# Optimization experiments

Hardware: AMD Instinct MI355X
Metric: run time of the kernel (lower is better)

Reference implementation:

```python
import jax, jax.numpy as jnp
import numpy as np

N_WAY = 5
K_SHOT = 1
QUERY = 75          # queries per class -> 375 total
PRJ = 14            # projections per support class
C, H, W = 512, 10, 10
NUM_NODE = H * W
SINK_EPS = 0.05     # entropic regularization (on max-normalized cost)
SINK_ITERS = 50


def setup_inputs() -> dict:
    key = jax.random.key(0)
    k1, k2 = jax.random.split(key)
    n_support = N_WAY * K_SHOT * PRJ
    num_query = N_WAY * QUERY
    feat = jax.random.normal(k1, (n_support + num_query, C, H, W), dtype=jnp.float32)
    label = jax.random.randint(k2, (num_query,), 0, N_WAY)
    return {"feat": feat, "label": label}


def _sinkhorn(cost, r, c, eps=SINK_EPS, iters=SINK_ITERS):
    """Batched entropic OT (log-domain Sinkhorn), replacing the per-pair
    cv2.EMD CPU solve. cost: [..., n, m]; r: [..., n]; c: [..., m].
    r and c each sum to NUM_NODE, so total transported mass is NUM_NODE,
    matching the cv2.EMD flow scale. Scaling the cost by a positive scalar
    does not change the (exact-)OT plan, so we max-normalize per pair for a
    consistent effective regularization."""
    scale = jnp.max(cost, axis=(-1, -2), keepdims=True) + 1e-6
    cost = cost / scale
    log_r = jnp.log(r)
    log_c = jnp.log(c)

    def body(fg, _):
        f, g = fg
        f = eps * (log_r - jax.nn.logsumexp((g[..., None, :] - cost) / eps, axis=-1))
        g = eps * (log_c - jax.nn.logsumexp((f[..., :, None] - cost) / eps, axis=-2))
        return (f, g), None

    init = (jnp.zeros_like(r), jnp.zeros_like(c))
    (f, g), _ = jax.lax.scan(body, init, None, length=iters)
    return jnp.exp((f[..., :, None] + g[..., None, :] - cost) / eps)


def reference(feat, label):
    n_support = N_WAY * K_SHOT * PRJ
    support = feat[:n_support].reshape(N_WAY, PRJ, C, H, W)
    query = feat[n_support:]                       # [nq, C, H, W]
    proto = support.mean(axis=1)                   # [way, C, H, W]
    nq = query.shape[0]

    # --- get_weight_vector: <A_node_feat, global_avg(B)> per (A,B) pair ---
    proto_avg = proto.mean(axis=(2, 3))            # [way, C]
    query_avg = query.mean(axis=(2, 3))            # [nq, C]
    qf = query.reshape(nq, C, NUM_NODE)
    pf = proto.reshape(N_WAY, C, NUM_NODE)
    w1 = jax.nn.relu(jnp.einsum('mcp,nc->mnp', qf, proto_avg)) + 0.001  # [nq, way, N]
    w2 = jax.nn.relu(jnp.einsum('ncp,mc->nmp', pf, query_avg)) + 0.001  # [way, nq, N]

    # --- normalize_feature: subtract channel mean ---
    protoN = proto - proto.mean(axis=1, keepdims=True)
    queryN = query - query.mean(axis=1, keepdims=True)

    # --- similarity map: 1 - squared L2 over channels, per node pair ---
    p = protoN.reshape(N_WAY, C, NUM_NODE).transpose(0, 2, 1)  # [way, N, C]
    q = queryN.reshape(nq, C, NUM_NODE).transpose(0, 2, 1)     # [nq, N, C]
    qn = (q ** 2).sum(-1)                                      # [nq, N]
    pn = (p ** 2).sum(-1)                                      # [way, N]
    cross = jnp.einsum('iac,jbc->ijab', q, p)                  # [nq, way, N, N]
    sqd = qn[:, None, :, None] + pn[None, :, None, :] - 2.0 * cross
    sim = 1.0 - sqd                                            # similarity_map
    cost = sqd                                                 # = 1 - sim

    # --- marginal weights, normalized to sum NUM_NODE (as in emd_inference) ---
    ww1 = jax.nn.relu(w1) + 1e-5
    ww1 = ww1 * (NUM_NODE / ww1.sum(-1, keepdims=True))        # [nq, way, N]
    ww2 = jax.nn.relu(jnp.transpose(w2, (1, 0, 2))) + 1e-5     # weight_2[j,i] -> [nq, way, N]
    ww2 = ww2 * (NUM_NODE / ww2.sum(-1, keepdims=True))

    # --- OT flow (detached, like torch.from_numpy(flow)) ---
    flow = jax.lax.stop_gradient(
        _sinkhorn(jax.lax.stop_gradient(cost), jax.lax.stop_gradient(ww1), jax.lax.stop_gradient(ww2))
    )

    temperature = 12.5 / NUM_NODE
    logits = (sim * flow).sum((-1, -2)) * temperature          # [nq, way]
    log_p_y = jax.nn.log_softmax(logits, axis=1)
    loss = -jnp.take_along_axis(log_p_y, label[:, None], axis=1).mean()
    return (log_p_y, loss)
```

## Files before the change

### kernel.cpp

```cpp
#include <hip/hip_runtime.h>
#include <math.h>

#define NW   5
#define PRJ  14
#define CCH  512
#define PP   100
#define NQ   375
#define NS   70
#define NPAIR (NQ*NW)

#define OFF_PROTO   0
#define OFF_PAVG    256000
#define OFF_QAVG    258560
#define OFF_QSQ     450560
#define OFF_PSQ     488060
#define OFF_LOGITS  488560
#define OFF_PF16    490440
#define OFF_AUX     654280
#define OFF_KG      1036780
#define OFF_QF16    19786844
#define REQ1_WS_BYTES ((size_t)(OFF_KG + 18750000 + 64) * 4)
#define REQ2_WS_BYTES ((size_t)(OFF_QF16 + 12288000 + 64) * 4)

typedef float f32x16 __attribute__((ext_vector_type(16)));
typedef _Float16 f16x2 __attribute__((ext_vector_type(2)));
typedef _Float16 f16x8 __attribute__((ext_vector_type(8)));

__device__ __forceinline__ int SWZ(int n) { return n ^ ((n >> 2) & 7); }

__global__ void k_proto(const float* __restrict__ feat, float* __restrict__ ws) {
    int nc = blockIdx.x;
    int n  = nc >> 9;
    int p  = threadIdx.x;
    float s = 0.f;
    if (p < PP) {
        const float* base = feat + (size_t)((n * PRJ) * CCH) * PP + (size_t)(nc & 511) * PP + p;
        #pragma unroll
        for (int k = 0; k < PRJ; ++k) s += base[(size_t)k * CCH * PP];
        s *= (1.f / PRJ);
        ws[OFF_PROTO + nc * PP + p] = s;
    }
    float v = (p < PP) ? s : 0.f;
    #pragma unroll
    for (int off = 32; off; off >>= 1) v += __shfl_down(v, off);
    __shared__ float red[2];
    if ((threadIdx.x & 63) == 0) red[threadIdx.x >> 6] = v;
    __syncthreads();
    if (threadIdx.x == 0) ws[OFF_PAVG + nc] = (red[0] + red[1]) * (1.f / PP);
}

__global__ __launch_bounds__(256) void k_qstat(const float* __restrict__ src,
                                               float* __restrict__ dst_sq,
                                               float* __restrict__ dst_avg) {
    __shared__ __align__(16) float t[6400];
    int b = blockIdx.x, tid = threadIdx.x;
    const float* base = src + (size_t)b * CCH * PP;
    float qsq = 0.f;
    for (int c0 = 0; c0 < CCH; c0 += 64) {
        __syncthreads();
        const float4* g = (const float4*)(base + (size_t)c0 * PP);
        for (int i = tid; i < 1600; i += 256) ((float4*)t)[i] = g[i];
        __syncthreads();
        if (tid < PP) {
            #pragma unroll 8
            for (int c = 0; c < 64; ++c) { float x = t[c * PP + tid]; qsq = fmaf(x, x, qsq); }
        } else if (tid >= 128 && tid < 192) {
            int ch = tid - 128;
            const float4* row = (const float4*)(t + ch * PP);
            float s = 0.f;
            #pragma unroll
            for (int i = 0; i < 25; ++i) { float4 v = row[i]; s += (v.x + v.y) + (v.z + v.w); }
            if (dst_avg) dst_avg[(size_t)b * CCH + c0 + ch] = s * (1.f / PP);
        }
    }
    if (tid < PP) dst_sq[b * PP + tid] = qsq;
}

__global__ __launch_bounds__(256) void k_conv(const float* __restrict__ src,
                                              const float* __restrict__ avg,
                                              uint* __restrict__ dst) {
    int b = blockIdx.x;
    int id = b >> 4, kt = b & 15;
    int tid = threadIdx.x;
    int c0 = kt * 32;
    uint* img = dst + (size_t)b * 2048;
    const float* pb = src + (size_t)id * CCH * PP;
    const float* pavg = avg + (size_t)id * CCH;
    for (int i = tid; i < 1600; i += 256) {
        int cp = i / 100, col = i - cp * 100;
        float a0 = pb[(size_t)(c0 + 2 * cp) * PP + col];
        float a1 = pb[(size_t)(c0 + 2 * cp + 1) * PP + col];
        uint pk = __builtin_bit_cast(uint, __builtin_amdgcn_cvt_pkrtz(a0, a1));
        img[(((cp >> 2) << 7) | SWZ(col)) * 4 + (cp & 3)] = pk;
    }
    if (tid < 16) {
        int cp = tid;
        float a0 = pavg[c0 + 2 * cp], a1 = pavg[c0 + 2 * cp + 1];
        uint pk = __builtin_bit_cast(uint, __builtin_amdgcn_cvt_pkrtz(a0, a1));
        img[(((cp >> 2) << 7) | 101) * 4 + (cp & 3)] = pk;
    }
    for (int i = tid; i < 448; i += 256) {
        int dw = i & 3; int t2 = i >> 2;
        int s_i = t2 % 28; int k4 = t2 / 28;
        int s = 100 + s_i;
        if (s == 101) continue;
        img[(((k4) << 7) | s) * 4 + dw] = (s == 100) ? 0x3C003C00u : 0u;
    }
}


__global__ __launch_bounds__(256, 4) void k_cost2(float* __restrict__ ws) {
    __shared__ __align__(16) char SH[22400];
    __shared__ float wrL[PP], wcL[PP], qnl[PP], pnl[PP], sqv[PP], spv[PP];
    __shared__ float red[8];
    uint* Kst = (uint*)SH;

    int p_ = blockIdx.x;
    int xcd = p_ & 7, off_ = p_ >> 3;
    int pair = (xcd < 3) ? (xcd * 235 + off_) : (705 + (xcd - 3) * 234 + off_);

    int m = pair / NW;
    int n = pair - m * NW;
    int tid = threadIdx.x;
    int lane = tid & 63, wid = tid >> 6;
    int lrow = lane & 31, lhi = lane >> 5;

    const char* qimg = (const char*)((const uint*)(ws + OFF_QF16) + (size_t)m * 16 * 2048);
    const char* pimg = (const char*)((const uint*)(ws + OFF_PF16) + (size_t)n * 16 * 2048);

    f32x16 acc[4];
    #pragma unroll
    for (int tc = 0; tc < 4; ++tc)
        #pragma unroll
        for (int e = 0; e < 16; ++e) acc[tc][e] = 0.f;

    int arow16 = SWZ(32 * wid + lrow) * 16;
    int bcol16[4];
    #pragma unroll
    for (int tc = 0; tc < 4; ++tc) bcol16[tc] = SWZ(32 * tc + lrow) * 16;

    #pragma unroll 2
    for (int kt = 0; kt < 16; ++kt) {
        const char* qk = qimg + kt * 8192;
        const char* pk = pimg + kt * 8192;
        #pragma unroll
        for (int s = 0; s < 2; ++s) {
            int kb = (2 * s + lhi) * 2048;
            f16x8 ah = *(const f16x8*)(qk + kb + arow16);
            f16x8 b0 = *(const f16x8*)(pk + kb + bcol16[0]);
            f16x8 b1 = *(const f16x8*)(pk + kb + bcol16[1]);
            f16x8 b2 = *(const f16x8*)(pk + kb + bcol16[2]);
            f16x8 b3 = *(const f16x8*)(pk + kb + bcol16[3]);
            acc[0] = __builtin_amdgcn_mfma_f32_32x32x16_f16(ah, b0, acc[0], 0, 0, 0);
            acc[1] = __builtin_amdgcn_mfma_f32_32x32x16_f16(ah, b1, acc[1], 0, 0, 0);
            acc[2] = __builtin_amdgcn_mfma_f32_32x32x16_f16(ah, b2, acc[2], 0, 0, 0);
            acc[3] = __builtin_amdgcn_mfma_f32_32x32x16_f16(ah, b3, acc[3], 0, 0, 0);
        }
    }

    if ((lane & 31) == 4 || (lane & 31) == 5) {
        float* dst = ((lane & 31) == 4) ? wrL : sqv;
        #pragma unroll
        for (int reg = 0; reg < 16; ++reg) {
            int row = 32 * wid + (reg & 3) + 8 * (reg >> 2) + 4 * lhi;
            if (row < PP) dst[row] = acc[3][reg];
        }
    }
    if (wid == 3 && lhi == 1) {
        #pragma unroll
        for (int tc = 0; tc < 4; ++tc) {
            int col = 32 * tc + lrow;
            if (col < PP) { wcL[col] = acc[tc][0]; spv[col] = acc[tc][1]; }
        }
    }
    __syncthreads();

    float v1 = 0.f, v2 = 0.f;
    if (tid < PP) {
        v1 = fmaxf(wrL[tid], 0.f) + 0.00101f;
        v2 = fmaxf(wcL[tid], 0.f) + 0.00101f;
    }
    float s1 = v1, s2 = v2;
    #pragma unroll
    for (int off = 32; off; off >>= 1) { s1 += __shfl_down(s1, off); s2 += __shfl_down(s2, off); }
    if ((tid & 63) == 0) { red[tid >> 6] = s1; red[4 + (tid >> 6)] = s2; }
    __syncthreads();
    float t1 = red[0] + red[1], t2 = red[4] + red[5];
    if (tid < PP) {
        wrL[tid] = v1 * (100.f / t1) * 4.f;
        wcL[tid] = v2 * (100.f / t2) * 4.f;
        float sq = sqv[tid], sp = spv[tid];
        qnl[tid] = ws[OFF_QSQ + m * PP + tid] - sq * sq * (1.f / 512.f);
        pnl[tid] = ws[OFF_PSQ + n * PP + tid] - sp * sp * (1.f / 512.f);
    }
    __syncthreads();

    float spc[4], pnc[4];
    #pragma unroll
    for (int tc = 0; tc < 4; ++tc) {
        int col = 32 * tc + lrow;
        bool cv = col < PP;
        spc[tc] = cv ? spv[col] : 0.f;
        pnc[tc] = cv ? pnl[col] : 0.f;
    }
    float mymax = -1e30f;
    #pragma unroll
    for (int reg = 0; reg < 16; ++reg) {
        int row = 32 * wid + (reg & 3) + 8 * (reg >> 2) + 4 * lhi;
        bool rv = row < PP;
        float sqr = rv ? sqv[row] : 0.f;
        float qnr = rv ? qnl[row] : 0.f;
        #pragma unroll
        for (int tc = 0; tc < 4; ++tc) {
            float sqd = qnr + pnc[tc] - 2.f * (acc[tc][reg] - sqr * spc[tc] * (1.f / 512.f));
            acc[tc][reg] = sqd;
            int col = 32 * tc + lrow;
            if (rv && col < PP) mymax = fmaxf(mymax, sqd);
        }
    }
    #pragma unroll
    for (int off = 32; off; off >>= 1) mymax = fmaxf(mymax, __shfl_down(mymax, off));
    __syncthreads();
    if (lane == 0) red[wid] = mymax;
    __syncthreads();
    float scale = fmaxf(fmaxf(red[0], red[1]), fmaxf(red[2], red[3])) + 1e-6f;
    float k2 = (1.f / scale) * (20.f * 1.44269504088896f);

    #pragma unroll
    for (int tc = 0; tc < 4; ++tc) {
        float kv[16];
        #pragma unroll
        for (int reg = 0; reg < 16; ++reg) kv[reg] = exp2f(fmaf(-acc[tc][reg], k2, 15.f));
        int col = 32 * tc + lrow;
        #pragma unroll
        for (int reg = 0; reg < 16; ++reg) {
            float pv = __shfl_xor(kv[reg], 1);
            int row = 32 * wid + (reg & 3) + 8 * (reg >> 2) + 4 * lhi;
            if (!(lane & 1) && row < PP && col < PP) {
                int j = col >> 1;
                int dw = (j < 25) ? j : (j + 3);
                uint pk = __builtin_bit_cast(uint, __builtin_amdgcn_cvt_pkrtz(kv[reg], pv));
                Kst[row * 56 + dw] = pk;
            }
        }
    }
    __syncthreads();

    int r_ = tid >> 1, hf = tid & 1;
    bool sact = tid < 200;
    if (sact) {
        uint Kr[25], KTr[25];
        const uint* rp = Kst + r_ * 56 + 28 * hf;
        #pragma unroll
        for (int q = 0; q < 25; ++q) Kr[q] = rp[q];
        int j = r_ >> 1;
        int dwc = (j < 25) ? j : (j + 3);
        int sh = (r_ & 1) * 16;
        const uint* cp0 = Kst + (50 * hf) * 56 + dwc;
        #pragma unroll
        for (int q = 0; q < 25; ++q) {
            uint d0 = cp0[(2 * q) * 56];
            uint d1 = cp0[(2 * q + 1) * 56];
            KTr[q] = ((d0 >> sh) & 0xFFFFu) | (((d1 >> sh) & 0xFFFFu) << 16);
        }
        uint* kg = (uint*)(ws + OFF_KG) + (size_t)pair * 10000 + (r_ >> 1);
        int ibR = (r_ & 1) * 50 + 25 * hf;
        int ibT = 100 + (r_ & 1) * 50 + 25 * hf;
        #pragma unroll
        for (int q = 0; q < 25; ++q) kg[(ibR + q) * 50] = Kr[q];
        #pragma unroll
        for (int q = 0; q < 25; ++q) kg[(ibT + q) * 50] = KTr[q];
    }
    float* aux = ws + OFF_AUX + (size_t)pair * 204;
    if (tid < PP) { aux[tid] = wrL[tid]; aux[100 + tid] = wcL[tid]; }
    if (tid == 0) aux[200] = scale;
}

__global__ __launch_bounds__(256, 4) void k_costL(const float* __restrict__ query,
                                                  float* __restrict__ ws) {
    __shared__ __align__(16) char SH[22400];
    __shared__ float wrL[PP], wcL[PP], qnl[PP], pnl[PP], sqv[PP], spv[PP];
    __shared__ float red[8];
    uint* Kst = (uint*)SH;

    int p_ = blockIdx.x;
    int xcd = p_ & 7, off_ = p_ >> 3;
    int pair = (xcd < 3) ? (xcd * 235 + off_) : (705 + (xcd - 3) * 234 + off_);

    int m = pair / NW;
    int n = pair - m * NW;
    int tid = threadIdx.x;
    int lane = tid & 63, wid = tid >> 6;
    int lrow = lane & 31, lhi = lane >> 5;

    const float* qb = query + (size_t)m * CCH * PP;
    const float* qavg_g = ws + OFF_QAVG + (size_t)m * CCH;
    const uint* pimg = (const uint*)(ws + OFF_PF16) + (size_t)n * 16 * 2048;

    for (int idx = tid; idx < 112; idx += 256) {
        int s_i = idx % 28; int k4 = idx / 28;
        int s = 100 + s_i;
        if (s == 101) continue;
        uint4 val = (s == 100)
                  ? make_uint4(0x3C003C00u, 0x3C003C00u, 0x3C003C00u, 0x3C003C00u)
                  : make_uint4(0u, 0u, 0u, 0u);
        *(uint4*)&SH[(k4 * 128 + s) * 16] = val;
    }

    f32x16 acc[4];
    #pragma unroll
    for (int tc = 0; tc < 4; ++tc)
        #pragma unroll
        for (int e = 0; e < 16; ++e) acc[tc][e] = 0.f;

    int arow16 = SWZ(32 * wid + lrow) * 16;
    int bcol16[4];
    #pragma unroll
    for (int tc = 0; tc < 4; ++tc) bcol16[tc] = SWZ(32 * tc + lrow) * 16;

    for (int kt = 0; kt < 16; ++kt) {
        int c0 = kt * 32;
        for (int idx = tid; idx < 400; idx += 256) {
            int cp = idx / 25, n4 = idx - cp * 25;
            const float* src = qb + (size_t)(c0 + 2 * cp) * PP + n4 * 4;
            float4 x0 = *(const float4*)src;
            float4 x1 = *(const float4*)(src + PP);
            const float* p0 = (const float*)&x0;
            const float* p1 = (const float*)&x1;
            int basedw = ((cp >> 2) << 7);
            int dwb = (cp & 3) * 4;
            #pragma unroll
            for (int i4 = 0; i4 < 4; ++i4) {
                int node = n4 * 4 + i4;
                uint pk = __builtin_bit_cast(uint, __builtin_amdgcn_cvt_pkrtz(p0[i4], p1[i4]));
                *(uint*)&SH[(basedw + SWZ(node)) * 16 + dwb] = pk;
            }
        }
        if (tid < 16) {
            int cp = tid;
            uint pk = __builtin_bit_cast(uint,
                __builtin_amdgcn_cvt_pkrtz(qavg_g[c0 + 2 * cp], qavg_g[c0 + 2 * cp + 1]));
            *(uint*)&SH[(((cp >> 2) << 7) + 101) * 16 + (cp & 3) * 4] = pk;
        }
        {
            const float4* gB = (const float4*)(pimg + (size_t)kt * 2048);
            float4* sB = (float4*)&SH[8192];
            for (int i = tid; i < 512; i += 256) sB[i] = gB[i];
        }
        __syncthreads();
        __builtin_amdgcn_s_setprio(1);
        #pragma unroll
        for (int s = 0; s < 2; ++s) {
            int kb = (2 * s + lhi) * 2048;
            f16x8 ah = *(const f16x8*)&SH[kb + arow16];
            #pragma unroll
            for (int tc = 0; tc < 4; ++tc) {
                f16x8 bh = *(const f16x8*)&SH[8192 + kb + bcol16[tc]];
                acc[tc] = __builtin_amdgcn_mfma_f32_32x32x16_f16(ah, bh, acc[tc], 0, 0, 0);
            }
        }
        __builtin_amdgcn_s_setprio(0);
        __syncthreads();
    }

    if ((lane & 31) == 4 || (lane & 31) == 5) {
        float* dst = ((lane & 31) == 4) ? wrL : sqv;
        #pragma unroll
        for (int reg = 0; reg < 16; ++reg) {
            int row = 32 * wid + (reg & 3) + 8 * (reg >> 2) + 4 * lhi;
            if (row < PP) dst[row] = acc[3][reg];
        }
    }
    if (wid == 3 && lhi == 1) {
        #pragma unroll
        for (int tc = 0; tc < 4; ++tc) {
            int col = 32 * tc + lrow;
            if (col < PP) { wcL[col] = acc[tc][0]; spv[col] = acc[tc][1]; }
        }
    }
    __syncthreads();

    float v1 = 0.f, v2 = 0.f;
    if (tid < PP) {
        v1 = fmaxf(wrL[tid], 0.f) + 0.00101f;
        v2 = fmaxf(wcL[tid], 0.f) + 0.00101f;
    }
    float s1 = v1, s2 = v2;
    #pragma unroll
    for (int off = 32; off; off >>= 1) { s1 += __shfl_down(s1, off); s2 += __shfl_down(s2, off); }
    if ((tid & 63) == 0) { red[tid >> 6] = s1; red[4 + (tid >> 6)] = s2; }
    __syncthreads();
    float t1 = red[0] + red[1], t2 = red[4] + red[5];
    if (tid < PP) {
        wrL[tid] = v1 * (100.f / t1) * 4.f;
        wcL[tid] = v2 * (100.f / t2) * 4.f;
        float sq = sqv[tid], sp = spv[tid];
        qnl[tid] = ws[OFF_QSQ + m * PP + tid] - sq * sq * (1.f / 512.f);
        pnl[tid] = ws[OFF_PSQ + n * PP + tid] - sp * sp * (1.f / 512.f);
    }
    __syncthreads();

    float spc[4], pnc[4];
    #pragma unroll
    for (int tc = 0; tc < 4; ++tc) {
        int col = 32 * tc + lrow;
        bool cv = col < PP;
        spc[tc] = cv ? spv[col] : 0.f;
        pnc[tc] = cv ? pnl[col] : 0.f;
    }
    float mymax = -1e30f;
    #pragma unroll
    for (int reg = 0; reg < 16; ++reg) {
        int row = 32 * wid + (reg & 3) + 8 * (reg >> 2) + 4 * lhi;
        bool rv = row < PP;
        float sqr = rv ? sqv[row] : 0.f;
        float qnr = rv ? qnl[row] : 0.f;
        #pragma unroll
        for (int tc = 0; tc < 4; ++tc) {
            float sqd = qnr + pnc[tc] - 2.f * (acc[tc][reg] - sqr * spc[tc] * (1.f / 512.f));
            acc[tc][reg] = sqd;
            int col = 32 * tc + lrow;
            if (rv && col < PP) mymax = fmaxf(mymax, sqd);
        }
    }
    #pragma unroll
    for (int off = 32; off; off >>= 1) mymax = fmaxf(mymax, __shfl_down(mymax, off));
    __syncthreads();
    if (lane == 0) red[wid] = mymax;
    __syncthreads();
    float scale = fmaxf(fmaxf(red[0], red[1]), fmaxf(red[2], red[3])) + 1e-6f;
    float k2 = (1.f / scale) * (20.f * 1.44269504088896f);

    #pragma unroll
    for (int tc = 0; tc < 4; ++tc) {
        float kv[16];
        #pragma unroll
        for (int reg = 0; reg < 16; ++reg) kv[reg] = exp2f(fmaf(-acc[tc][reg], k2, 15.f));
        int col = 32 * tc + lrow;
        #pragma unroll
        for (int reg = 0; reg < 16; ++reg) {
            float pv = __shfl_xor(kv[reg], 1);
            int row = 32 * wid + (reg & 3) + 8 * (reg >> 2) + 4 * lhi;
            if (!(lane & 1) && row < PP && col < PP) {
                int j = col >> 1;
                int dw = (j < 25) ? j : (j + 3);
                uint pk = __builtin_bit_cast(uint, __builtin_amdgcn_cvt_pkrtz(kv[reg], pv));
                Kst[row * 56 + dw] = pk;
            }
        }
    }
    __syncthreads();

    int r_ = tid >> 1, hf = tid & 1;
    bool sact = tid < 200;
    if (sact) {
        uint Kr[25], KTr[25];
        const uint* rp = Kst + r_ * 56 + 28 * hf;
        #pragma unroll
        for (int q = 0; q < 25; ++q) Kr[q] = rp[q];
        int j = r_ >> 1;
        int dwc = (j < 25) ? j : (j + 3);
        int sh = (r_ & 1) * 16;
        const uint* cp0 = Kst + (50 * hf) * 56 + dwc;
        #pragma unroll
        for (int q = 0; q < 25; ++q) {
            uint d0 = cp0[(2 * q) * 56];
            uint d1 = cp0[(2 * q + 1) * 56];
            KTr[q] = ((d0 >> sh) & 0xFFFFu) | (((d1 >> sh) & 0xFFFFu) << 16);
        }
        uint* kg = (uint*)(ws + OFF_KG) + (size_t)pair * 10000 + (r_ >> 1);
        int ibR = (r_ & 1) * 50 + 25 * hf;
        int ibT = 100 + (r_ & 1) * 50 + 25 * hf;
        #pragma unroll
        for (int q = 0; q < 25; ++q) kg[(ibR + q) * 50] = Kr[q];
        #pragma unroll
        for (int q = 0; q < 25; ++q) kg[(ibT + q) * 50] = KTr[q];
    }
    float* aux = ws + OFF_AUX + (size_t)pair * 204;
    if (tid < PP) { aux[tid] = wrL[tid]; aux[100 + tid] = wcL[tid]; }
    if (tid == 0) aux[200] = scale;
}

__global__ __launch_bounds__(64, 2) void k_sink(float* __restrict__ ws) {
    __shared__ __align__(16) uint uhL[52], vhL[52];
    int pair = blockIdx.x;
    int l = threadIdx.x;
    bool act = l < 50;

    const float* aux = ws + OFF_AUX + (size_t)pair * 204;
    float wr0 = 0.f, wr1 = 0.f, wc0 = 0.f, wc1 = 0.f;
    if (act) {
        wr0 = aux[2 * l]; wr1 = aux[2 * l + 1];
        wc0 = aux[100 + 2 * l]; wc1 = aux[101 + 2 * l];
    }
    float scale = aux[200];
    float rk2 = scale * (1.f / (20.f * 1.44269504088896f));

    uint K0[50], K1[50], T0[50], T1[50];
    {
        const uint* kg = (const uint*)(ws + OFF_KG) + (size_t)pair * 10000 + (l < 50 ? l : 0);
        #pragma unroll
        for (int i = 0; i < 50; ++i) K0[i] = kg[i * 50];
        #pragma unroll
        for (int i = 0; i < 50; ++i) K1[i] = kg[(50 + i) * 50];
        #pragma unroll
        for (int i = 0; i < 50; ++i) T0[i] = kg[(100 + i) * 50];
        #pragma unroll
        for (int i = 0; i < 50; ++i) T1[i] = kg[(150 + i) * 50];
    }
    if (l < 52) { vhL[l] = (l < 50) ? 0x3C003C00u : 0u; uhL[l] = 0u; }
    __syncthreads();

    float u0 = 0.f, u1 = 0.f;
    for (int it = 0; it < 50; ++it) {
        if (act) {
            const uint4* vp4 = (const uint4*)vhL;
            float a0 = 0.f, b0 = 0.f, a1 = 0.f, b1 = 0.f;
            #pragma unroll
            for (int d4 = 0; d4 < 12; ++d4) {
                uint4 V = vp4[d4];
                a0 = __builtin_amdgcn_fdot2(__builtin_bit_cast(f16x2, K0[4*d4+0]), __builtin_bit_cast(f16x2, V.x), a0, false);
                b0 = __builtin_amdgcn_fdot2(__builtin_bit_cast(f16x2, K0[4*d4+1]), __builtin_bit_cast(f16x2, V.y), b0, false);
                a0 = __builtin_amdgcn_fdot2(__builtin_bit_cast(f16x2, K0[4*d4+2]), __builtin_bit_cast(f16x2, V.z), a0, false);
                b0 = __builtin_amdgcn_fdot2(__builtin_bit_cast(f16x2, K0[4*d4+3]), __builtin_bit_cast(f16x2, V.w), b0, false);
                a1 = __builtin_amdgcn_fdot2(__builtin_bit_cast(f16x2, K1[4*d4+0]), __builtin_bit_cast(f16x2, V.x), a1, false);
                b1 = __builtin_amdgcn_fdot2(__builtin_bit_cast(f16x2, K1[4*d4+1]), __builtin_bit_cast(f16x2, V.y), b1, false);
                a1 = __builtin_amdgcn_fdot2(__builtin_bit_cast(f16x2, K1[4*d4+2]), __builtin_bit_cast(f16x2, V.z), a1, false);
                b1 = __builtin_amdgcn_fdot2(__builtin_bit_cast(f16x2, K1[4*d4+3]), __builtin_bit_cast(f16x2, V.w), b1, false);
            }
            {
                uint v48 = vhL[48], v49 = vhL[49];
                a0 = __builtin_amdgcn_fdot2(__builtin_bit_cast(f16x2, K0[48]), __builtin_bit_cast(f16x2, v48), a0, false);
                b0 = __builtin_amdgcn_fdot2(__builtin_bit_cast(f16x2, K0[49]), __builtin_bit_cast(f16x2, v49), b0, false);
                a1 = __builtin_amdgcn_fdot2(__builtin_bit_cast(f16x2, K1[48]), __builtin_bit_cast(f16x2, v48), a1, false);
                b1 = __builtin_amdgcn_fdot2(__builtin_bit_cast(f16x2, K1[49]), __builtin_bit_cast(f16x2, v49), b1, false);
            }
            u0 = fminf(wr0 * __builtin_amdgcn_rcpf(a0 + b0), 60000.f);
            u1 = fminf(wr1 * __builtin_amdgcn_rcpf(a1 + b1), 60000.f);
            uhL[l] = __builtin_bit_cast(uint, __builtin_amdgcn_cvt_pkrtz(u0, u1));
        }
        __syncthreads();
        if (act) {
            const uint4* up4 = (const uint4*)uhL;
            float a0 = 0.f, b0 = 0.f, a1 = 0.f, b1 = 0.f;
            #pragma unroll
            for (int d4 = 0; d4 < 12; ++d4) {
                uint4 U = up4[d4];
                a0 = __builtin_amdgcn_fdot2(__builtin_bit_cast(f16x2, T0[4*d4+0]), __builtin_bit_cast(f16x2, U.x), a0, false);
                b0 = __builtin_amdgcn_fdot2(__builtin_bit_cast(f16x2, T0[4*d4+1]), __builtin_bit_cast(f16x2, U.y), b0, false);
                a0 = __builtin_amdgcn_fdot2(__builtin_bit_cast(f16x2, T0[4*d4+2]), __builtin_bit_cast(f16x2, U.z), a0, false);
                b0 = __builtin_amdgcn_fdot2(__builtin_bit_cast(f16x2, T0[4*d4+3]), __builtin_bit_cast(f16x2, U.w), b0, false);
                a1 = __builtin_amdgcn_fdot2(__builtin_bit_cast(f16x2, T1[4*d4+0]), __builtin_bit_cast(f16x2, U.x), a1, false);
                b1 = __builtin_amdgcn_fdot2(__builtin_bit_cast(f16x2, T1[4*d4+1]), __builtin_bit_cast(f16x2, U.y), b1, false);
                a1 = __builtin_amdgcn_fdot2(__builtin_bit_cast(f16x2, T1[4*d4+2]), __builtin_bit_cast(f16x2, U.z), a1, false);
                b1 = __builtin_amdgcn_fdot2(__builtin_bit_cast(f16x2, T1[4*d4+3]), __builtin_bit_cast(f16x2, U.w), b1, false);
            }
            {
                uint u48 = uhL[48], u49 = uhL[49];
                a0 = __builtin_amdgcn_fdot2(__builtin_bit_cast(f16x2, T0[48]), __builtin_bit_cast(f16x2, u48), a0, false);
                b0 = __builtin_amdgcn_fdot2(__builtin_bit_cast(f16x2, T0[49]), __builtin_bit_cast(f16x2, u49), b0, false);
                a1 = __builtin_amdgcn_fdot2(__builtin_bit_cast(f16x2, T1[48]), __builtin_bit_cast(f16x2, u48), a1, false);
                b1 = __builtin_amdgcn_fdot2(__builtin_bit_cast(f16x2, T1[49]), __builtin_bit_cast(f16x2, u49), b1, false);
            }
            float v0 = fminf(wc0 * __builtin_amdgcn_rcpf(a0 + b0), 60000.f);
            float v1n = fminf(wc1 * __builtin_amdgcn_rcpf(a1 + b1), 60000.f);
            vhL[l] = __builtin_bit_cast(uint, __builtin_amdgcn_cvt_pkrtz(v0, v1n));
        }
        __syncthreads();
    }

    float lsum = 0.f;
    if (act) {
        float l0 = 0.f, l1 = 0.f;
        #pragma unroll
        for (int d = 0; d < 50; ++d) {
            f16x2 vv = __builtin_bit_cast(f16x2, vhL[d]);
            f16x2 h0 = __builtin_bit_cast(f16x2, K0[d]);
            f16x2 h1 = __builtin_bit_cast(f16x2, K1[d]);
            float k00 = (float)h0[0], k01 = (float)h0[1];
            float k10 = (float)h1[0], k11 = (float)h1[1];
            float v0 = (float)vv[0], v1v = (float)vv[1];
            l0 = fmaf((1.f - (15.f - __log2f(k00)) * rk2) * k00, v0, l0);
            l0 = fmaf((1.f - (15.f - __log2f(k01)) * rk2) * k01, v1v, l0);
            l1 = fmaf((1.f - (15.f - __log2f(k10)) * rk2) * k10, v0, l1);
            l1 = fmaf((1.f - (15.f - __log2f(k11)) * rk2) * k11, v1v, l1);
        }
        lsum = l0 * u0 + l1 * u1;
    }
    #pragma unroll
    for (int off = 32; off; off >>= 1) lsum += __shfl_down(lsum, off);
    if (l == 0) ws[OFF_LOGITS + pair] = lsum * (0.125f / 4.f);
}

__global__ void k_final(const int* __restrict__ label, const float* __restrict__ ws,
                        float* __restrict__ out) {
    int t = threadIdx.x;
    float contrib = 0.f;
    if (t < NQ) {
        float lg[NW];
        #pragma unroll
        for (int n = 0; n < NW; ++n) lg[n] = ws[OFF_LOGITS + t * NW + n];
        float mx = lg[0];
        #pragma unroll
        for (int n = 1; n < NW; ++n) mx = fmaxf(mx, lg[n]);
        float s = 0.f;
        #pragma unroll
        for (int n = 0; n < NW; ++n) s += expf(lg[n] - mx);
        float lse = mx + logf(s);
        int lab = label[t];
        #pragma unroll
        for (int n = 0; n < NW; ++n) {
            float lp = lg[n] - lse;
            out[t * NW + n] = lp;
            if (n == lab) contrib = -lp;
        }
    }
    #pragma unroll
    for (int off = 32; off; off >>= 1) contrib += __shfl_down(contrib, off);
    __shared__ float red[6];
    if ((t & 63) == 0) red[t >> 6] = contrib;
    __syncthreads();
    if (t == 0) {
        float s = 0.f;
        #pragma unroll
        for (int i = 0; i < 6; ++i) s += red[i];
        out[NQ * NW] = s * (1.f / NQ);
    }
}

extern "C" void kernel_launch(void* const* d_in, const int* in_sizes, int n_in,
                              void* d_out, int out_size, void* d_ws, size_t ws_size,
                              hipStream_t stream) {
    const float* feat  = (const float*)d_in[0];
    const int*   label = (const int*)d_in[1];
    float* out = (float*)d_out;
    float* ws  = (float*)d_ws;
    const float* query = feat + (size_t)NS * CCH * PP;

    k_proto<<<NW * CCH, 128, 0, stream>>>(feat, ws);
    k_qstat<<<NQ, 256, 0, stream>>>(query, ws + OFF_QSQ, ws + OFF_QAVG);
    k_qstat<<<NW, 256, 0, stream>>>(ws + OFF_PROTO, ws + OFF_PSQ, (float*)nullptr);
    k_conv<<<NW * 16, 256, 0, stream>>>(ws + OFF_PROTO, ws + OFF_PAVG, (uint*)(ws + OFF_PF16));
    if (ws_size >= REQ2_WS_BYTES) {
        k_conv<<<NQ * 16, 256, 0, stream>>>(query, ws + OFF_QAVG, (uint*)(ws + OFF_QF16));
        k_cost2<<<NPAIR, 256, 0, stream>>>(ws);
        k_sink<<<NPAIR, 64, 0, stream>>>(ws);
    } else {
        k_costL<<<NPAIR, 256, 0, stream>>>(query, ws);
        k_sink<<<NPAIR, 64, 0, stream>>>(ws);
    }
    k_final<<<1, 384, 0, stream>>>(label, ws, out);
}
```

Before: 232.9 us.

## Fuse query fp16 packing into stats pass and coalesce K matrix layout

The query fp16 swizzled image is now written from the shared-memory tile already staged in k_qstat, so the separate k_conv pass no longer re-reads the full query tensor from global memory. A small k_qpad kernel fills only the avg and padding slots. The K/KT workspace layout is also changed so k_cost2 writes contiguous rows and k_sink loads uint2 pairs with lane-contiguous addresses instead of strided scalar loads. This adds more work and more global stores to k_qstat, and it introduces a new layout contract between the cost and sink kernels.

```diff
diff --git a/kernel.cpp b/kernel.cpp
--- a/kernel.cpp
+++ b/kernel.cpp
@@ -19,7 +19,6 @@
 #define OFF_AUX     654280
 #define OFF_KG      1036780
 #define OFF_QF16    19786844
-#define REQ1_WS_BYTES ((size_t)(OFF_KG + 18750000 + 64) * 4)
 #define REQ2_WS_BYTES ((size_t)(OFF_QF16 + 12288000 + 64) * 4)
 
 typedef float f32x16 __attribute__((ext_vector_type(16)));
@@ -51,10 +50,12 @@
 
 __global__ __launch_bounds__(256) void k_qstat(const float* __restrict__ src,
                                                float* __restrict__ dst_sq,
-                                               float* __restrict__ dst_avg) {
+                                               float* __restrict__ dst_avg,
+                                               uint* __restrict__ qimg) {
     __shared__ __align__(16) float t[6400];
     int b = blockIdx.x, tid = threadIdx.x;
     const float* base = src + (size_t)b * CCH * PP;
+    uint* imgb = qimg ? (qimg + (size_t)b * 32768) : (uint*)0;
     float qsq = 0.f;
     for (int c0 = 0; c0 < CCH; c0 += 64) {
         __syncthreads();
@@ -72,8 +73,41 @@
             for (int i = 0; i < 25; ++i) { float4 v = row[i]; s += (v.x + v.y) + (v.z + v.w); }
             if (dst_avg) dst_avg[(size_t)b * CCH + c0 + ch] = s * (1.f / PP);
         }
+        if (imgb) {
+            for (int i = tid; i < 3200; i += 256) {
+                int cpl = i / 100, col = i - cpl * 100;
+                int cp = (c0 >> 1) + cpl;
+                int kt = cp >> 4, cpk = cp & 15;
+                float a0 = t[(2 * cpl) * 100 + col];
+                float a1 = t[(2 * cpl + 1) * 100 + col];
+                uint pk = __builtin_bit_cast(uint, __builtin_amdgcn_cvt_pkrtz(a0, a1));
+                imgb[(size_t)kt * 2048 + ((((cpk >> 2) << 7) | SWZ(col)) * 4 + (cpk & 3))] = pk;
+            }
+        }
     }
     if (tid < PP) dst_sq[b * PP + tid] = qsq;
+}
+
+__global__ __launch_bounds__(256) void k_qpad(const float* __restrict__ avg,
+                                              uint* __restrict__ dst) {
+    int b = blockIdx.x;
+    int tid = threadIdx.x;
+    uint* img = dst + (size_t)b * 32768;
+    const float* av = avg + (size_t)b * CCH;
+    if (tid < 256) {
+        int kt = tid >> 4, cp = tid & 15;
+        float a0 = av[kt * 32 + 2 * cp], a1 = av[kt * 32 + 2 * cp + 1];
+        uint pk = __builtin_bit_cast(uint, __builtin_amdgcn_cvt_pkrtz(a0, a1));
+        img[(size_t)kt * 2048 + (((cp >> 2) << 7) | 101) * 4 + (cp & 3)] = pk;
+    }
+    for (int i = tid; i < 6912; i += 256) {
+        int dw = i & 3; int t2 = i >> 2;
+        int k4 = t2 & 3; int t3 = t2 >> 2;
+        int s_i = t3 % 27; int kt = t3 / 27;
+        int s = 100 + s_i + (s_i >= 1 ? 1 : 0);
+        uint val = (s == 100) ? 0x3C003C00u : 0u;
+        img[(size_t)kt * 2048 + (((k4) << 7) | s) * 4 + dw] = val;
+    }
 }
 
 __global__ __launch_bounds__(256) void k_conv(const float* __restrict__ src,
@@ -108,7 +142,6 @@
     }
 }
 
-
 __global__ __launch_bounds__(256, 4) void k_cost2(float* __restrict__ ws) {
     __shared__ __align__(16) char SH[22400];
     __shared__ float wrL[PP], wcL[PP], qnl[PP], pnl[PP], sqv[PP], spv[PP];
@@ -263,13 +296,11 @@
             uint d1 = cp0[(2 * q + 1) * 56];
             KTr[q] = ((d0 >> sh) & 0xFFFFu) | (((d1 >> sh) & 0xFFFFu) << 16);
         }
-        uint* kg = (uint*)(ws + OFF_KG) + (size_t)pair * 10000 + (r_ >> 1);
-        int ibR = (r_ & 1) * 50 + 25 * hf;
-        int ibT = 100 + (r_ & 1) * 50 + 25 * hf;
-        #pragma unroll
-        for (int q = 0; q < 25; ++q) kg[(ibR + q) * 50] = Kr[q];
-        #pragma unroll
-        for (int q = 0; q < 25; ++q) kg[(ibT + q) * 50] = KTr[q];
+        uint* kg = (uint*)(ws + OFF_KG) + (size_t)pair * 10000;
+        #pragma unroll
+        for (int q = 0; q < 25; ++q) kg[(25 * hf + q) * 100 + r_] = Kr[q];
+        #pragma unroll
+        for (int q = 0; q < 25; ++q) kg[5000 + (25 * hf + q) * 100 + r_] = KTr[q];
     }
     float* aux = ws + OFF_AUX + (size_t)pair * 204;
     if (tid < PP) { aux[tid] = wrL[tid]; aux[100 + tid] = wcL[tid]; }
@@ -468,13 +499,11 @@
             uint d1 = cp0[(2 * q + 1) * 56];
             KTr[q] = ((d0 >> sh) & 0xFFFFu) | (((d1 >> sh) & 0xFFFFu) << 16);
         }
-        uint* kg = (uint*)(ws + OFF_KG) + (size_t)pair * 10000 + (r_ >> 1);
-        int ibR = (r_ & 1) * 50 + 25 * hf;
-        int ibT = 100 + (r_ & 1) * 50 + 25 * hf;
-        #pragma unroll
-        for (int q = 0; q < 25; ++q) kg[(ibR + q) * 50] = Kr[q];
-        #pragma unroll
-        for (int q = 0; q < 25; ++q) kg[(ibT + q) * 50] = KTr[q];
+        uint* kg = (uint*)(ws + OFF_KG) + (size_t)pair * 10000;
+        #pragma unroll
+        for (int q = 0; q < 25; ++q) kg[(25 * hf + q) * 100 + r_] = Kr[q];
+        #pragma unroll
+        for (int q = 0; q < 25; ++q) kg[5000 + (25 * hf + q) * 100 + r_] = KTr[q];
     }
     float* aux = ws + OFF_AUX + (size_t)pair * 204;
     if (tid < PP) { aux[tid] = wrL[tid]; aux[100 + tid] = wcL[tid]; }
@@ -498,15 +527,12 @@
 
     uint K0[50], K1[50], T0[50], T1[50];
     {
-        const uint* kg = (const uint*)(ws + OFF_KG) + (size_t)pair * 10000 + (l < 50 ? l : 0);
-        #pragma unroll
-        for (int i = 0; i < 50; ++i) K0[i] = kg[i * 50];
-        #pragma unroll
-        for (int i = 0; i < 50; ++i) K1[i] = kg[(50 + i) * 50];
-        #pragma unroll
-        for (int i = 0; i < 50; ++i) T0[i] = kg[(100 + i) * 50];
-        #pragma unroll
-        for (int i = 0; i < 50; ++i) T1[i] = kg[(150 + i) * 50];
+        const uint2* kg2 = (const uint2*)((const uint*)(ws + OFF_KG) + (size_t)pair * 10000);
+        int ll = act ? l : 0;
+        #pragma unroll
+        for (int j = 0; j < 50; ++j) { uint2 kk = kg2[j * 50 + ll]; K0[j] = kk.x; K1[j] = kk.y; }
+        #pragma unroll
+        for (int j = 0; j < 50; ++j) { uint2 kk = kg2[2500 + j * 50 + ll]; T0[j] = kk.x; T1[j] = kk.y; }
     }
     if (l < 52) { vhL[l] = (l < 50) ? 0x3C003C00u : 0u; uhL[l] = 0u; }
     __syncthreads();
@@ -636,13 +662,15 @@
     float* out = (float*)d_out;
     float* ws  = (float*)d_ws;
     const float* query = feat + (size_t)NS * CCH * PP;
+    bool fast = ws_size >= REQ2_WS_BYTES;
 
     k_proto<<<NW * CCH, 128, 0, stream>>>(feat, ws);
-    k_qstat<<<NQ, 256, 0, stream>>>(query, ws + OFF_QSQ, ws + OFF_QAVG);
-    k_qstat<<<NW, 256, 0, stream>>>(ws + OFF_PROTO, ws + OFF_PSQ, (float*)nullptr);
+    k_qstat<<<NQ, 256, 0, stream>>>(query, ws + OFF_QSQ, ws + OFF_QAVG,
+                                    fast ? (uint*)(ws + OFF_QF16) : (uint*)0);
+    k_qstat<<<NW, 256, 0, stream>>>(ws + OFF_PROTO, ws + OFF_PSQ, (float*)0, (uint*)0);
     k_conv<<<NW * 16, 256, 0, stream>>>(ws + OFF_PROTO, ws + OFF_PAVG, (uint*)(ws + OFF_PF16));
-    if (ws_size >= REQ2_WS_BYTES) {
-        k_conv<<<NQ * 16, 256, 0, stream>>>(query, ws + OFF_QAVG, (uint*)(ws + OFF_QF16));
+    if (fast) {
+        k_qpad<<<NQ, 256, 0, stream>>>(ws + OFF_QAVG, (uint*)(ws + OFF_QF16));
         k_cost2<<<NPAIR, 256, 0, stream>>>(ws);
         k_sink<<<NPAIR, 64, 0, stream>>>(ws);
     } else {
```

Measured after the change: 226.8 us. -2.6%, faster.
